# Kernel tuning notes

Hardware: AMD Instinct MI355X
Metric: run time of the kernel (lower is better)

Reference implementation:

```python
import jax, jax.numpy as jnp
import numpy as np

B, T, V, H = 512, 1024, 27, 512  # batch, seq, N+1 vocab, hidden


def setup_inputs() -> dict:
    key = jax.random.key(0)
    ks = jax.random.split(key, 7)
    s_ih = 1.0 / np.sqrt(H)
    return {
        "x": jax.random.uniform(ks[0], (B, T, V), dtype=jnp.float32),
        "W_ih": jax.random.normal(ks[1], (3 * H, V), dtype=jnp.float32) * s_ih,
        "W_hh": jax.random.normal(ks[2], (3 * H, H), dtype=jnp.float32) * s_ih,
        "b_ih": jax.random.normal(ks[3], (3 * H,), dtype=jnp.float32) * s_ih,
        "b_hh": jax.random.normal(ks[4], (3 * H,), dtype=jnp.float32) * s_ih,
        "W_dec": jax.random.normal(ks[5], (V, H), dtype=jnp.float32) * s_ih,
        "b_dec": jax.random.normal(ks[6], (V,), dtype=jnp.float32) * s_ih,
    }


def reference(x, W_ih, W_hh, b_ih, b_hh, W_dec, b_dec):
    # x: (B, T, V). Precompute the input projection for all timesteps at once.
    gi_all = jnp.einsum("btv,gv->btg", x, W_ih) + b_ih  # (B, T, 3H)
    h0 = jnp.zeros((x.shape[0], W_hh.shape[1]), dtype=x.dtype)

    def step(h, gi_t):
        gh = h @ W_hh.T + b_hh                       # (B, 3H)
        i_r, i_z, i_n = jnp.split(gi_t, 3, axis=-1)
        h_r, h_z, h_n = jnp.split(gh, 3, axis=-1)
        r = jax.nn.sigmoid(i_r + h_r)
        z = jax.nn.sigmoid(i_z + h_z)
        n = jnp.tanh(i_n + r * h_n)
        h_new = (1.0 - z) * n + z * h                # torch GRUCell update
        return h_new, h_new

    _, hs = jax.lax.scan(step, h0, jnp.swapaxes(gi_all, 0, 1))  # hs: (T, B, H)
    hs = jnp.swapaxes(hs, 0, 1)                                  # (B, T, H)
    logits = jnp.einsum("bth,vh->btv", hs, W_dec) + b_dec        # per-step decode
    return logits
```

## Files before the change

### kernel.cpp

```cpp
#include <hip/hip_runtime.h>
#include <math.h>

#define Bsz 512
#define Tsz 1024
#define Vsz 27
#define Hsz 512
#define BH (Bsz * Hsz)
#define TV (Tsz * Vsz)
#define NBLK 256
#define NT 256
#define JB 32

typedef float f32x4 __attribute__((ext_vector_type(4)));
typedef short s16x8 __attribute__((ext_vector_type(8)));
typedef unsigned int u32x4 __attribute__((ext_vector_type(4)));
#define MFMA __builtin_amdgcn_mfma_f32_16x16x32_bf16

#define WS_CNT  ((size_t)2 * 3 * BH * 2)
#define WS_FLG  (WS_CNT + 4096)
#define WS_DSTG (WS_FLG + 262144)
#define WS_WXG  (WS_DSTG + (size_t)2 * 16 * 512 * 2)

__device__ __forceinline__ unsigned short btrunc(float x) {
    return (unsigned short)(__float_as_uint(x) >> 16);
}
__device__ __forceinline__ float bup(unsigned short b) {
    return __uint_as_float(((unsigned)b) << 16);
}
__device__ __forceinline__ unsigned short brne(float x) {
    unsigned u = __float_as_uint(x);
    return (unsigned short)((u + 0x7FFFu + ((u >> 16) & 1u)) >> 16);
}
__device__ __forceinline__ __amdgpu_buffer_rsrc_t make_rsrc(void* p, unsigned bytes) {
    return __builtin_amdgcn_make_buffer_rsrc(p, (short)0, (int)bytes, 0x00020000);
}
template<bool FAST>
__device__ __forceinline__ s16x8 loadA(__amdgpu_buffer_rsrc_t r, int off) {
    u32x4 d = __builtin_amdgcn_raw_buffer_load_b128(r, off, 0, FAST ? 0 : 0x11);
    return __builtin_bit_cast(s16x8, d);
}
template<bool FAST>
__device__ __forceinline__ void storeH(__amdgpu_buffer_rsrc_t r, int off, unsigned short v) {
    __builtin_amdgcn_raw_buffer_store_b16(v, r, off, 0, FAST ? 0 : 0x11);
}
__device__ __forceinline__ unsigned* flag_ptr(unsigned* flags, int bt, int m, int jp) {
    return flags + (size_t)((((bt << 2) + m) << 5) + jp) * 32;
}

#define TRI6(AR, AZ, AN, R1,R2,R3, Z1,Z2,Z3, N1,N2,N3, A1_,A2_,A3_) do { \
    AR = MFMA(A1_, R1, AR,0,0,0); AZ = MFMA(A1_, Z1, AZ,0,0,0); AN = MFMA(A1_, N1, AN,0,0,0); \
    AR = MFMA(A1_, R2, AR,0,0,0); AZ = MFMA(A1_, Z2, AZ,0,0,0); AN = MFMA(A1_, N2, AN,0,0,0); \
    AR = MFMA(A2_, R1, AR,0,0,0); AZ = MFMA(A2_, Z1, AZ,0,0,0); AN = MFMA(A2_, N1, AN,0,0,0); \
    AR = MFMA(A1_, R3, AR,0,0,0); AZ = MFMA(A1_, Z3, AZ,0,0,0); AN = MFMA(A1_, N3, AN,0,0,0); \
    AR = MFMA(A2_, R2, AR,0,0,0); AZ = MFMA(A2_, Z2, AZ,0,0,0); AN = MFMA(A2_, N2, AN,0,0,0); \
    AR = MFMA(A3_, R1, AR,0,0,0); AZ = MFMA(A3_, Z1, AZ,0,0,0); AN = MFMA(A3_, N1, AN,0,0,0); \
} while (0)
#define TRI5(AR, AZ, AN, R1,R2, Z1,Z2, N1,N2, A1_,A2_,A3_) do { \
    AR = MFMA(A1_, R1, AR,0,0,0); AZ = MFMA(A1_, Z1, AZ,0,0,0); AN = MFMA(A1_, N1, AN,0,0,0); \
    AR = MFMA(A1_, R2, AR,0,0,0); AZ = MFMA(A1_, Z2, AZ,0,0,0); AN = MFMA(A1_, N2, AN,0,0,0); \
    AR = MFMA(A2_, R1, AR,0,0,0); AZ = MFMA(A2_, Z1, AZ,0,0,0); AN = MFMA(A2_, N1, AN,0,0,0); \
    AR = MFMA(A2_, R2, AR,0,0,0); AZ = MFMA(A2_, Z2, AZ,0,0,0); AN = MFMA(A2_, N2, AN,0,0,0); \
    AR = MFMA(A3_, R1, AR,0,0,0); AZ = MFMA(A3_, Z1, AZ,0,0,0); AN = MFMA(A3_, N1, AN,0,0,0); \
} while (0)

__global__ void init_ws_kernel(unsigned short* __restrict__ hpl, unsigned* __restrict__ cntr,
                               unsigned short* __restrict__ Dstg, unsigned short* __restrict__ Wxg,
                               const float* __restrict__ W_ih, const float* __restrict__ W_dec)
{
    size_t gid = (size_t)blockIdx.x * 256 + threadIdx.x;
    size_t gsz = (size_t)gridDim.x * 256;
    for (size_t i = gid; i < (size_t)(2 * 3 * BH * 2) / 16; i += gsz)
        ((uint4*)hpl)[i] = make_uint4(0u, 0u, 0u, 0u);
    for (size_t i = gid; i < 33792; i += gsz) cntr[i] = 0u;
    for (size_t i = gid; i < 2 * 16 * 512; i += gsz) {
        int e = i & 7, ln2 = (i >> 3) & 63, c = (i >> 9) & 15, jj = (int)(i >> 13);
        int cc2 = ln2 & 15, qq2 = ln2 >> 4;
        int k = c * 32 + qq2 * 8 + e;
        int vr = jj * 16 + cc2;
        Dstg[i] = (vr < Vsz) ? brne(W_dec[(size_t)vr * Hsz + k]) : (unsigned short)0;
    }
    for (size_t i = gid; i < 1536 * 64; i += gsz) {
        int k = i & 31, p = (i >> 5) & 1, grow = (int)(i >> 6);
        float v = (k < Vsz) ? W_ih[grow * Vsz + k] : 0.f;
        unsigned short t1 = btrunc(v); float r1 = v - bup(t1);
        unsigned short t2 = btrunc(r1);
        Wxg[i] = p ? t2 : t1;
    }
}

__device__ __forceinline__ void group_barrier(unsigned* c, unsigned target) {
    __syncthreads();
    if (threadIdx.x == 0) {
        __hip_atomic_fetch_add(c, 1u, __ATOMIC_RELAXED, __HIP_MEMORY_SCOPE_AGENT);
        while (__hip_atomic_load(c, __ATOMIC_RELAXED, __HIP_MEMORY_SCOPE_AGENT) < target)
            __builtin_amdgcn_s_sleep(2);
    }
    __syncthreads();
}

template<bool FAST>
__device__ __forceinline__ void gru_loop(
    const float* __restrict__ x, float* __restrict__ out,
    const unsigned short* __restrict__ Dstg, const unsigned short* __restrict__ Wxg,
    unsigned* __restrict__ flags, __amdgpu_buffer_rsrc_t hrs,
    const unsigned short* Bst,
    float bih_r, float bih_z, float bih_n,
    float bhh_r, float bhh_z, float bhh_n, float bdv,
    int tid, int bt, int j, int b0, int g0)
{
    const int w = tid >> 6, ln = tid & 63;
    const int m = w;
    const int cc = ln & 15, qq = ln >> 4;
    const int arow = b0 + (m << 4) + cc;
    const int rowBase = (arow * Hsz + (qq << 3)) << 1;
    unsigned* myflag = flag_ptr(flags, bt, m, j);
    unsigned* gateP  = flag_ptr(flags, bt, m, ln & 31);
    const int vcol = (j << 4) + cc;

    float hk[4] = {0.f, 0.f, 0.f, 0.f};

    for (int i = 0; i <= Tsz; ++i) {
        if (FAST) asm volatile("buffer_inv" ::: "memory");
        float xreg[8];
        if (i < Tsz) {
            #pragma unroll
            for (int e = 0; e < 8; ++e) {
                int k = (qq << 3) + e;
                xreg[e] = (k < Vsz) ? x[(size_t)arow * TV + (size_t)i * Vsz + k] : 0.f;
            }
        }

        for (;;) {
            unsigned v = __hip_atomic_load(gateP, __ATOMIC_RELAXED, __HIP_MEMORY_SCOPE_AGENT);
            if (__all((int)v >= i)) break;
        }

        const int voffA0 = (i & 1) * (3 * BH * 2) + rowBase;

        s16x8 A1s[16], A2s[16], A3s[16];
        #pragma unroll
        for (int c = 0; c < 16; ++c) {
            A1s[c] = loadA<FAST>(hrs, voffA0 + c * 64);
            A2s[c] = loadA<FAST>(hrs, voffA0 + c * 64 + BH * 2);
            A3s[c] = loadA<FAST>(hrs, voffA0 + c * 64 + 2 * BH * 2);
        }

        f32x4 accR = {0,0,0,0}, accZ = {0,0,0,0}, accNh = {0,0,0,0};
        f32x4 accNi = {0,0,0,0}, accD = {0,0,0,0};

        #pragma unroll
        for (int c = 0; c < 16; ++c) {
            const unsigned short* bs = Bst + (size_t)(c * 9) * 512 + (ln << 3);
            s16x8 R1 = *(const s16x8*)(bs);
            s16x8 R2 = *(const s16x8*)(bs + 512);
            s16x8 R3 = *(const s16x8*)(bs + 1024);
            s16x8 Z1 = *(const s16x8*)(bs + 1536);
            s16x8 Z2 = *(const s16x8*)(bs + 2048);
            s16x8 Z3 = *(const s16x8*)(bs + 2560);
            s16x8 N1 = *(const s16x8*)(bs + 3072);
            s16x8 N2 = *(const s16x8*)(bs + 3584);
            s16x8 N3 = *(const s16x8*)(bs + 4096);
            TRI6(accR, accZ, accNh, R1,R2,R3, Z1,Z2,Z3, N1,N2,N3,
                 A1s[c], A2s[c], A3s[c]);
            if (j < 2) {
                s16x8 D1 = *(const s16x8*)(Dstg + (size_t)((j << 4) + c) * 512 + (ln << 3));
                accD = MFMA(A1s[c], D1, accD, 0, 0, 0);
                accD = MFMA(A2s[c], D1, accD, 0, 0, 0);
            }
        }

        if (i < Tsz) {
            s16x8 A1, A2, A3;
            #pragma unroll
            for (int e = 0; e < 8; ++e) {
                float v = xreg[e];
                unsigned short s1 = btrunc(v); float r1 = v - bup(s1);
                unsigned short s2 = btrunc(r1); float r2 = r1 - bup(s2);
                unsigned short s3 = btrunc(r2);
                A1[e] = (short)s1; A2[e] = (short)s2; A3[e] = (short)s3;
            }
            const unsigned short* wr = Wxg + (size_t)(g0 + cc) * 64 + (qq << 3);
            const unsigned short* wz = Wxg + (size_t)(Hsz + g0 + cc) * 64 + (qq << 3);
            const unsigned short* wn = Wxg + (size_t)(2 * Hsz + g0 + cc) * 64 + (qq << 3);
            s16x8 Br1 = *(const s16x8*)(wr), Br2 = *(const s16x8*)(wr + 32);
            s16x8 Bz1 = *(const s16x8*)(wz), Bz2 = *(const s16x8*)(wz + 32);
            s16x8 Bn1 = *(const s16x8*)(wn), Bn2 = *(const s16x8*)(wn + 32);
            TRI5(accR, accZ, accNi, Br1,Br2, Bz1,Bz2, Bn1,Bn2, A1, A2, A3);
        }

        if (i < Tsz) {
            const int wpar = ((i + 1) & 1) * (3 * BH * 2);
            #pragma unroll
            for (int r = 0; r < 4; ++r) {
                float rv = accR[r] + bih_r + bhh_r;
                float zv = accZ[r] + bih_z + bhh_z;
                float nh = accNh[r] + bhh_n;
                float ni = accNi[r] + bih_n;
                float rg = 1.f / (1.f + expf(-rv));
                float zg = 1.f / (1.f + expf(-zv));
                float ng = tanhf(ni + rg * nh);
                float hv = (1.f - zg) * ng + zg * hk[r];
                hk[r] = hv;
                int brow = b0 + (m << 4) + (qq << 2) + r;
                int e2 = wpar + ((brow * Hsz + g0 + cc) << 1);
                unsigned short s1 = btrunc(hv); float r1 = hv - bup(s1);
                unsigned short s2 = btrunc(r1); float r2 = r1 - bup(s2);
                unsigned short s3 = btrunc(r2);
                storeH<FAST>(hrs, e2, s1);
                storeH<FAST>(hrs, e2 + BH * 2, s2);
                storeH<FAST>(hrs, e2 + 2 * BH * 2, s3);
            }
        }
        if (i < Tsz) {
            asm volatile("s_waitcnt vmcnt(0)" ::: "memory");
            if (ln == 0)
                __hip_atomic_store(myflag, (unsigned)(i + 1), __ATOMIC_RELAXED,
                                   __HIP_MEMORY_SCOPE_AGENT);
        }
        if (i > 0 && j < 2 && vcol < Vsz) {
            #pragma unroll
            for (int r = 0; r < 4; ++r) {
                size_t brow = (size_t)(b0 + (m << 4) + (qq << 2) + r);
                out[brow * TV + (size_t)(i - 1) * Vsz + vcol] = accD[r] + bdv;
            }
        }
    }
}

__global__ __launch_bounds__(NT, 1) void gru_persist(
    const float* __restrict__ x, const float* __restrict__ W_ih,
    const float* __restrict__ W_hh, const float* __restrict__ b_ih,
    const float* __restrict__ b_hh, const float* __restrict__ W_dec,
    const float* __restrict__ b_dec, char* __restrict__ wsb,
    float* __restrict__ out)
{
    __shared__ unsigned short Bst[16 * 9 * 512];
    __shared__ int fastFlag;

    unsigned short* hpl = (unsigned short*)wsb;
    unsigned* cbase = (unsigned*)(wsb + WS_CNT);
    unsigned* flags = (unsigned*)(wsb + WS_FLG);
    unsigned short* Dstg = (unsigned short*)(wsb + WS_DSTG);
    unsigned short* Wxg  = (unsigned short*)(wsb + WS_WXG);

    const int tid = threadIdx.x;
    const int bt  = blockIdx.x & 7;
    const int j   = blockIdx.x >> 3;
    const int b0  = bt * 64;
    const int g0  = j * 16;
    unsigned* pcnt  = cbase + 16 + bt;
    unsigned* xmask = cbase + 32 + bt;

    for (int idx = tid; idx < 16 * 9 * 512; idx += NT) {
        int e = idx & 7, ln2 = (idx >> 3) & 63, s = idx >> 9;
        int p = s % 3, t = (s / 3) % 3, c = s / 9;
        int cc2 = ln2 & 15, qq2 = ln2 >> 4;
        int k = c * 32 + qq2 * 8 + e;
        int grow = t * Hsz + g0 + cc2;
        float v = W_hh[(size_t)grow * Hsz + k];
        unsigned short t1 = btrunc(v); float r1 = v - bup(t1);
        unsigned short t2 = btrunc(r1); float r2 = r1 - bup(t2);
        unsigned short t3 = btrunc(r2);
        Bst[idx] = (p == 0) ? t1 : (p == 1) ? t2 : t3;
    }
    if (tid == 0) {
        unsigned xcc;
        asm volatile("s_getreg_b32 %0, hwreg(20, 0, 32)" : "=s"(xcc));
        __hip_atomic_fetch_or(xmask, 1u << (xcc & 31), __ATOMIC_RELAXED,
                              __HIP_MEMORY_SCOPE_AGENT);
        asm volatile("s_waitcnt vmcnt(0)" ::: "memory");
    }
    group_barrier(pcnt, JB);
    if (tid == 0) {
        unsigned f = __hip_atomic_load(xmask, __ATOMIC_RELAXED, __HIP_MEMORY_SCOPE_AGENT);
        fastFlag = (__popc(f) == 1) ? 1 : 0;
    }
    __syncthreads();
    const bool fastv = (fastFlag != 0);

    const int cc = tid & 15;
    const float bih_r = b_ih[g0 + cc];
    const float bih_z = b_ih[Hsz + g0 + cc];
    const float bih_n = b_ih[2 * Hsz + g0 + cc];
    const float bhh_r = b_hh[g0 + cc];
    const float bhh_z = b_hh[Hsz + g0 + cc];
    const float bhh_n = b_hh[2 * Hsz + g0 + cc];
    const int vcol = (j << 4) + cc;
    const float bdv = (j < 2 && vcol < Vsz) ? b_dec[vcol] : 0.f;
    __amdgpu_buffer_rsrc_t hrs = make_rsrc((void*)hpl, (unsigned)(2u * 3u * BH * 2u));

    if (fastv)
        gru_loop<true>(x, out, Dstg, Wxg, flags, hrs, Bst,
                       bih_r, bih_z, bih_n, bhh_r, bhh_z, bhh_n, bdv,
                       tid, bt, j, b0, g0);
    else
        gru_loop<false>(x, out, Dstg, Wxg, flags, hrs, Bst,
                        bih_r, bih_z, bih_n, bhh_r, bhh_z, bhh_n, bdv,
                        tid, bt, j, b0, g0);
}

extern "C" void kernel_launch(void* const* d_in, const int* in_sizes, int n_in,
                              void* d_out, int out_size, void* d_ws, size_t ws_size,
                              hipStream_t stream) {
    const float* x     = (const float*)d_in[0];
    const float* W_ih  = (const float*)d_in[1];
    const float* W_hh  = (const float*)d_in[2];
    const float* b_ih  = (const float*)d_in[3];
    const float* b_hh  = (const float*)d_in[4];
    const float* W_dec = (const float*)d_in[5];
    const float* b_dec = (const float*)d_in[6];
    float* out = (float*)d_out;
    char* wsb  = (char*)d_ws;

    init_ws_kernel<<<768, 256, 0, stream>>>(
        (unsigned short*)wsb, (unsigned*)(wsb + WS_CNT),
        (unsigned short*)(wsb + WS_DSTG), (unsigned short*)(wsb + WS_WXG),
        W_ih, W_dec);

    gru_persist<<<dim3(NBLK), dim3(NT), 0, stream>>>(
        x, W_ih, W_hh, b_ih, b_hh, W_dec, b_dec, wsb, out);
}
```

Before: 12.03 ms.

## Halve block threads, give each wave two row tiles with double-buffered h loads

Cuts the block from 4 waves to 2, and each wave now handles two 16-row batch tiles. The shared-memory W_hh fragments are loaded once and reused for both tiles. The hidden-state A-fragment loads are now double-buffered per k-chunk instead of all 48 being fetched up front, which lowers register pressure and overlaps global loads with MFMAs. The cost is fewer waves per CU to hide latency and longer serial work per wave on the recurrent critical path. The flag and sync indexing by wave still uses m, so correctness depends on the unseen flag layout matching the new wave count.

```diff
diff --git a/kernel.cpp b/kernel.cpp
--- a/kernel.cpp
+++ b/kernel.cpp
@@ -8,7 +8,7 @@
 #define BH (Bsz * Hsz)
 #define TV (Tsz * Vsz)
 #define NBLK 256
-#define NT 256
+#define NT 128
 #define JB 32
 
 typedef float f32x4 __attribute__((ext_vector_type(4)));
@@ -111,22 +111,26 @@
     const int w = tid >> 6, ln = tid & 63;
     const int m = w;
     const int cc = ln & 15, qq = ln >> 4;
-    const int arow = b0 + (m << 4) + cc;
-    const int rowBase = (arow * Hsz + (qq << 3)) << 1;
+    const int ar0 = b0 + (m << 5) + cc;
+    const int ar1 = ar0 + 16;
+    const int rb0 = (ar0 * Hsz + (qq << 3)) << 1;
+    const int rb1 = (ar1 * Hsz + (qq << 3)) << 1;
     unsigned* myflag = flag_ptr(flags, bt, m, j);
     unsigned* gateP  = flag_ptr(flags, bt, m, ln & 31);
     const int vcol = (j << 4) + cc;
 
-    float hk[4] = {0.f, 0.f, 0.f, 0.f};
+    float hk0[4] = {0.f, 0.f, 0.f, 0.f};
+    float hk1[4] = {0.f, 0.f, 0.f, 0.f};
 
     for (int i = 0; i <= Tsz; ++i) {
         if (FAST) asm volatile("buffer_inv" ::: "memory");
-        float xreg[8];
+        float xr0[8], xr1[8];
         if (i < Tsz) {
             #pragma unroll
             for (int e = 0; e < 8; ++e) {
                 int k = (qq << 3) + e;
-                xreg[e] = (k < Vsz) ? x[(size_t)arow * TV + (size_t)i * Vsz + k] : 0.f;
+                xr0[e] = (k < Vsz) ? x[(size_t)ar0 * TV + (size_t)i * Vsz + k] : 0.f;
+                xr1[e] = (k < Vsz) ? x[(size_t)ar1 * TV + (size_t)i * Vsz + k] : 0.f;
             }
         }
 
@@ -135,21 +139,32 @@
             if (__all((int)v >= i)) break;
         }
 
-        const int voffA0 = (i & 1) * (3 * BH * 2) + rowBase;
-
-        s16x8 A1s[16], A2s[16], A3s[16];
+        const int par = (i & 1) * (3 * BH * 2);
+        const int vA0 = par + rb0, vA1 = par + rb1;
+
+        f32x4 aR0 = {0,0,0,0}, aZ0 = {0,0,0,0}, aNh0 = {0,0,0,0};
+        f32x4 aR1 = {0,0,0,0}, aZ1 = {0,0,0,0}, aNh1 = {0,0,0,0};
+        f32x4 aNi0 = {0,0,0,0}, aNi1 = {0,0,0,0};
+        f32x4 aD0 = {0,0,0,0}, aD1 = {0,0,0,0};
+
+        s16x8 Pa1[2], Pa2[2], Pa3[2], Pb1[2], Pb2[2], Pb3[2];
+        Pa1[0] = loadA<FAST>(hrs, vA0);
+        Pa2[0] = loadA<FAST>(hrs, vA0 + BH * 2);
+        Pa3[0] = loadA<FAST>(hrs, vA0 + 2 * BH * 2);
+        Pb1[0] = loadA<FAST>(hrs, vA1);
+        Pb2[0] = loadA<FAST>(hrs, vA1 + BH * 2);
+        Pb3[0] = loadA<FAST>(hrs, vA1 + 2 * BH * 2);
         #pragma unroll
         for (int c = 0; c < 16; ++c) {
-            A1s[c] = loadA<FAST>(hrs, voffA0 + c * 64);
-            A2s[c] = loadA<FAST>(hrs, voffA0 + c * 64 + BH * 2);
-            A3s[c] = loadA<FAST>(hrs, voffA0 + c * 64 + 2 * BH * 2);
-        }
-
-        f32x4 accR = {0,0,0,0}, accZ = {0,0,0,0}, accNh = {0,0,0,0};
-        f32x4 accNi = {0,0,0,0}, accD = {0,0,0,0};
-
-        #pragma unroll
-        for (int c = 0; c < 16; ++c) {
+            const int cur = c & 1, nxt = cur ^ 1;
+            if (c < 15) {
+                Pa1[nxt] = loadA<FAST>(hrs, vA0 + (c + 1) * 64);
+                Pa2[nxt] = loadA<FAST>(hrs, vA0 + (c + 1) * 64 + BH * 2);
+                Pa3[nxt] = loadA<FAST>(hrs, vA0 + (c + 1) * 64 + 2 * BH * 2);
+                Pb1[nxt] = loadA<FAST>(hrs, vA1 + (c + 1) * 64);
+                Pb2[nxt] = loadA<FAST>(hrs, vA1 + (c + 1) * 64 + BH * 2);
+                Pb3[nxt] = loadA<FAST>(hrs, vA1 + (c + 1) * 64 + 2 * BH * 2);
+            }
             const unsigned short* bs = Bst + (size_t)(c * 9) * 512 + (ln << 3);
             s16x8 R1 = *(const s16x8*)(bs);
             s16x8 R2 = *(const s16x8*)(bs + 512);
@@ -160,55 +175,94 @@
             s16x8 N1 = *(const s16x8*)(bs + 3072);
             s16x8 N2 = *(const s16x8*)(bs + 3584);
             s16x8 N3 = *(const s16x8*)(bs + 4096);
-            TRI6(accR, accZ, accNh, R1,R2,R3, Z1,Z2,Z3, N1,N2,N3,
-                 A1s[c], A2s[c], A3s[c]);
+            TRI6(aR0, aZ0, aNh0, R1,R2,R3, Z1,Z2,Z3, N1,N2,N3,
+                 Pa1[cur], Pa2[cur], Pa3[cur]);
+            TRI6(aR1, aZ1, aNh1, R1,R2,R3, Z1,Z2,Z3, N1,N2,N3,
+                 Pb1[cur], Pb2[cur], Pb3[cur]);
             if (j < 2) {
                 s16x8 D1 = *(const s16x8*)(Dstg + (size_t)((j << 4) + c) * 512 + (ln << 3));
-                accD = MFMA(A1s[c], D1, accD, 0, 0, 0);
-                accD = MFMA(A2s[c], D1, accD, 0, 0, 0);
+                aD0 = MFMA(Pa1[cur], D1, aD0, 0, 0, 0);
+                aD0 = MFMA(Pa2[cur], D1, aD0, 0, 0, 0);
+                aD1 = MFMA(Pb1[cur], D1, aD1, 0, 0, 0);
+                aD1 = MFMA(Pb2[cur], D1, aD1, 0, 0, 0);
             }
         }
 
         if (i < Tsz) {
-            s16x8 A1, A2, A3;
-            #pragma unroll
-            for (int e = 0; e < 8; ++e) {
-                float v = xreg[e];
-                unsigned short s1 = btrunc(v); float r1 = v - bup(s1);
-                unsigned short s2 = btrunc(r1); float r2 = r1 - bup(s2);
-                unsigned short s3 = btrunc(r2);
-                A1[e] = (short)s1; A2[e] = (short)s2; A3[e] = (short)s3;
-            }
             const unsigned short* wr = Wxg + (size_t)(g0 + cc) * 64 + (qq << 3);
             const unsigned short* wz = Wxg + (size_t)(Hsz + g0 + cc) * 64 + (qq << 3);
             const unsigned short* wn = Wxg + (size_t)(2 * Hsz + g0 + cc) * 64 + (qq << 3);
             s16x8 Br1 = *(const s16x8*)(wr), Br2 = *(const s16x8*)(wr + 32);
             s16x8 Bz1 = *(const s16x8*)(wz), Bz2 = *(const s16x8*)(wz + 32);
             s16x8 Bn1 = *(const s16x8*)(wn), Bn2 = *(const s16x8*)(wn + 32);
-            TRI5(accR, accZ, accNi, Br1,Br2, Bz1,Bz2, Bn1,Bn2, A1, A2, A3);
+            {
+                s16x8 A1, A2, A3;
+                #pragma unroll
+                for (int e = 0; e < 8; ++e) {
+                    float v = xr0[e];
+                    unsigned short s1 = btrunc(v); float r1 = v - bup(s1);
+                    unsigned short s2 = btrunc(r1); float r2 = r1 - bup(s2);
+                    unsigned short s3 = btrunc(r2);
+                    A1[e] = (short)s1; A2[e] = (short)s2; A3[e] = (short)s3;
+                }
+                TRI5(aR0, aZ0, aNi0, Br1,Br2, Bz1,Bz2, Bn1,Bn2, A1, A2, A3);
+            }
+            {
+                s16x8 A1, A2, A3;
+                #pragma unroll
+                for (int e = 0; e < 8; ++e) {
+                    float v = xr1[e];
+                    unsigned short s1 = btrunc(v); float r1 = v - bup(s1);
+                    unsigned short s2 = btrunc(r1); float r2 = r1 - bup(s2);
+                    unsigned short s3 = btrunc(r2);
+                    A1[e] = (short)s1; A2[e] = (short)s2; A3[e] = (short)s3;
+                }
+                TRI5(aR1, aZ1, aNi1, Br1,Br2, Bz1,Bz2, Bn1,Bn2, A1, A2, A3);
+            }
         }
 
         if (i < Tsz) {
             const int wpar = ((i + 1) & 1) * (3 * BH * 2);
             #pragma unroll
             for (int r = 0; r < 4; ++r) {
-                float rv = accR[r] + bih_r + bhh_r;
-                float zv = accZ[r] + bih_z + bhh_z;
-                float nh = accNh[r] + bhh_n;
-                float ni = accNi[r] + bih_n;
-                float rg = 1.f / (1.f + expf(-rv));
-                float zg = 1.f / (1.f + expf(-zv));
-                float ng = tanhf(ni + rg * nh);
-                float hv = (1.f - zg) * ng + zg * hk[r];
-                hk[r] = hv;
-                int brow = b0 + (m << 4) + (qq << 2) + r;
-                int e2 = wpar + ((brow * Hsz + g0 + cc) << 1);
-                unsigned short s1 = btrunc(hv); float r1 = hv - bup(s1);
-                unsigned short s2 = btrunc(r1); float r2 = r1 - bup(s2);
-                unsigned short s3 = btrunc(r2);
-                storeH<FAST>(hrs, e2, s1);
-                storeH<FAST>(hrs, e2 + BH * 2, s2);
-                storeH<FAST>(hrs, e2 + 2 * BH * 2, s3);
+                {
+                    float rv = aR0[r] + bih_r + bhh_r;
+                    float zv = aZ0[r] + bih_z + bhh_z;
+                    float nh = aNh0[r] + bhh_n;
+                    float ni = aNi0[r] + bih_n;
+                    float rg = 1.f / (1.f + expf(-rv));
+                    float zg = 1.f / (1.f + expf(-zv));
+                    float ng = tanhf(ni + rg * nh);
+                    float hv = (1.f - zg) * ng + zg * hk0[r];
+                    hk0[r] = hv;
+                    int brow = b0 + (m << 5) + (qq << 2) + r;
+                    int e2 = wpar + ((brow * Hsz + g0 + cc) << 1);
+                    unsigned short s1 = btrunc(hv); float r1 = hv - bup(s1);
+                    unsigned short s2 = btrunc(r1); float r2 = r1 - bup(s2);
+                    unsigned short s3 = btrunc(r2);
+                    storeH<FAST>(hrs, e2, s1);
+                    storeH<FAST>(hrs, e2 + BH * 2, s2);
+                    storeH<FAST>(hrs, e2 + 2 * BH * 2, s3);
+                }
+                {
+                    float rv = aR1[r] + bih_r + bhh_r;
+                    float zv = aZ1[r] + bih_z + bhh_z;
+                    float nh = aNh1[r] + bhh_n;
+                    float ni = aNi1[r] + bih_n;
+                    float rg = 1.f / (1.f + expf(-rv));
+                    float zg = 1.f / (1.f + expf(-zv));
+                    float ng = tanhf(ni + rg * nh);
+                    float hv = (1.f - zg) * ng + zg * hk1[r];
+                    hk1[r] = hv;
+                    int brow = b0 + (m << 5) + 16 + (qq << 2) + r;
+                    int e2 = wpar + ((brow * Hsz + g0 + cc) << 1);
+                    unsigned short s1 = btrunc(hv); float r1 = hv - bup(s1);
+                    unsigned short s2 = btrunc(r1); float r2 = r1 - bup(s2);
+                    unsigned short s3 = btrunc(r2);
+                    storeH<FAST>(hrs, e2, s1);
+                    storeH<FAST>(hrs, e2 + BH * 2, s2);
+                    storeH<FAST>(hrs, e2 + 2 * BH * 2, s3);
+                }
             }
         }
         if (i < Tsz) {
@@ -220,8 +274,10 @@
         if (i > 0 && j < 2 && vcol < Vsz) {
             #pragma unroll
             for (int r = 0; r < 4; ++r) {
-                size_t brow = (size_t)(b0 + (m << 4) + (qq << 2) + r);
-                out[brow * TV + (size_t)(i - 1) * Vsz + vcol] = accD[r] + bdv;
+                size_t br0 = (size_t)(b0 + (m << 5) + (qq << 2) + r);
+                size_t br1 = br0 + 16;
+                out[br0 * TV + (size_t)(i - 1) * Vsz + vcol] = aD0[r] + bdv;
+                out[br1 * TV + (size_t)(i - 1) * Vsz + vcol] = aD1[r] + bdv;
             }
         }
     }
```

Measured after the change: 11.69 ms. -2.8%, faster.
